# Optimization experiments

Measured on AMD Instinct MI355X. Metric: run time of the kernel, lower is better.

The kernel has to match this reference:

```python
import jax, jax.numpy as jnp
import numpy as np

B, S, D, H, HD = 2, 2048, 1024, 16, 64


def setup_inputs() -> dict:
    key = jax.random.key(0)
    ks = jax.random.split(key, 11)
    scale_in = 1.0 / np.sqrt(D)
    return {
        "query": jax.random.normal(ks[0], (B, S, D), jnp.float32),
        "key": jax.random.normal(ks[1], (B, S, D), jnp.float32),
        "value": jax.random.normal(ks[2], (B, S, D), jnp.float32),
        "Wq": jax.random.normal(ks[3], (H, D, HD), jnp.float32) * scale_in,
        "bq": jax.random.normal(ks[4], (H, HD), jnp.float32) * 0.02,
        "Wk": jax.random.normal(ks[5], (H, D, HD), jnp.float32) * scale_in,
        "bk": jax.random.normal(ks[6], (H, HD), jnp.float32) * 0.02,
        "Wv": jax.random.normal(ks[7], (H, D, HD), jnp.float32) * scale_in,
        "bv": jax.random.normal(ks[8], (H, HD), jnp.float32) * 0.02,
        "Wo": jax.random.normal(ks[9], (D, D), jnp.float32) * scale_in,
        "bo": jax.random.normal(ks[10], (D,), jnp.float32) * 0.02,
    }


def reference(query, key, value, Wq, bq, Wk, bk, Wv, bv, Wo, bo):
    # Per-head projections, batched over heads (equivalent to the ModuleList loop).
    q = jnp.einsum('bsd,hdk->bhsk', query, Wq) + bq[None, :, None, :]   # [B,H,S,HD]
    k = jnp.einsum('bsd,hdk->bhsk', key, Wk) + bk[None, :, None, :]
    v = jnp.einsum('bsd,hdk->bhsk', value, Wv) + bv[None, :, None, :]
    scale = 1.0 / jnp.sqrt(jnp.asarray(q.shape[-1], q.dtype))
    scores = jnp.einsum('bhsk,bhtk->bhst', q, k) * scale                # [B,H,S,S]
    attn = jax.nn.softmax(scores, axis=-1)
    ctx = jnp.einsum('bhst,bhtk->bhsk', attn, v)                        # [B,H,S,HD]
    # Concat heads along last dim: [B,S,H*HD] == [B,S,D]
    x = jnp.transpose(ctx, (0, 2, 1, 3)).reshape(ctx.shape[0], ctx.shape[2], -1)
    return x @ Wo + bo
```

## Files before the change

kernel.cpp:

```cpp
#include <hip/hip_runtime.h>
#include <hip/hip_bf16.h>

typedef __bf16 bf16;
typedef __bf16 bf16x8 __attribute__((ext_vector_type(8)));
typedef __bf16 bf16x4 __attribute__((ext_vector_type(4)));
typedef __bf16 bf16x2 __attribute__((ext_vector_type(2)));
typedef float floatx4 __attribute__((ext_vector_type(4)));
typedef float floatx16 __attribute__((ext_vector_type(16)));
typedef int intx4 __attribute__((ext_vector_type(4)));

#define B_SZ 2
#define S_LEN 2048
#define D_DIM 1024
#define H_CNT 16
#define HD_DIM 64
#define M_ROWS 4096
#define QSCALE 0.18033688011112042f

__device__ __forceinline__ void async_ld16(const bf16* g, bf16* s) {
    __builtin_amdgcn_global_load_lds((const __attribute__((address_space(1))) void*)g,
                                     (__attribute__((address_space(3))) void*)s, 16, 0, 0);
}

__device__ __forceinline__ floatx4 mfma16(bf16x8 a, bf16x8 b, floatx4 c) {
    return __builtin_amdgcn_mfma_f32_16x16x32_bf16(a, b, c, 0, 0, 0);
}
__device__ __forceinline__ floatx16 mfma32(bf16x8 a, bf16x8 b, floatx16 c) {
    return __builtin_amdgcn_mfma_f32_32x32x16_bf16(a, b, c, 0, 0, 0);
}

__device__ __forceinline__ bf16x8 mkfrag(int a0, int a1, int b0, int b1) {
    asm("v_permlane32_swap_b32 %0, %1" : "+v"(a0), "+v"(b0));
    asm("v_permlane32_swap_b32 %0, %1" : "+v"(a1), "+v"(b1));
    intx4 q = {a0, a1, b0, b1};
    return __builtin_bit_cast(bf16x8, q);
}

struct PrepArgs {
    const float* cast_src[3]; bf16* cast_dst[3];
    const float* w_src[3];    bf16* w_dst[3];
    const float* wo;          bf16* wo_t;
};
__global__ __launch_bounds__(256) void prep(PrepArgs a) {
    __shared__ bf16 tile[32][33];
    const int bx = blockIdx.x, tid = threadIdx.x;
    if (bx < 12288) {
        const int t = bx >> 12, blk = bx & 4095;
        const float* s = a.cast_src[t];
        bf16* d = a.cast_dst[t];
        size_t i = ((size_t)blk * 256 + tid) * 4;
        float4 v = *(const float4*)(s + i);
        bf16x4 o = { (bf16)v.x, (bf16)v.y, (bf16)v.z, (bf16)v.w };
        *(bf16x4*)(d + i) = o;
        return;
    }
    int tx = tid & 31, ty = tid >> 5;
    const float* src; bf16* dst; int r0, c0, C, R;
    if (bx < 15360) {
        int idx = bx - 12288;
        int z = idx >> 6, xy = idx & 63;
        int mat = z >> 4, head = z & 15;
        src = a.w_src[mat] + (size_t)head * D_DIM * HD_DIM;
        dst = a.w_dst[mat] + (size_t)head * D_DIM * HD_DIM;
        r0 = (xy & 31) * 32; c0 = (xy >> 5) * 32; C = HD_DIM; R = D_DIM;
    } else {
        int idx = bx - 15360;
        src = a.wo; dst = a.wo_t;
        r0 = (idx & 31) * 32; c0 = (idx >> 5) * 32; C = D_DIM; R = D_DIM;
    }
#pragma unroll
    for (int i = 0; i < 32; i += 8)
        tile[ty + i][tx] = (bf16)src[(size_t)(r0 + ty + i) * C + c0 + tx];
    __syncthreads();
#pragma unroll
    for (int i = 0; i < 32; i += 8)
        dst[(size_t)(c0 + ty + i) * R + r0 + tx] = tile[tx][ty + i];
}

struct GemmPtrs { const bf16* A; const bf16* BT; const float* bias; bf16* C;
                  float scale; int mode; };
struct GemmArgs { GemmPtrs p[3]; };

__global__ __launch_bounds__(256) void gemm_bt(GemmArgs args) {
    __shared__ __align__(16) bf16 As[128 * 32];
    __shared__ __align__(16) bf16 Bs[128 * 32];
    const GemmPtrs P = args.p[blockIdx.z];
    const int tid = threadIdx.x, wave = tid >> 6, lane = tid & 63;
    const int quad = lane >> 4, l15 = lane & 15;
    const int bm = blockIdx.x * 128, bn = blockIdx.y * 128;
    const int wm = (wave >> 1) * 64, wn = (wave & 1) * 64;

    floatx4 acc[4][4];
#pragma unroll
    for (int i = 0; i < 4; i++)
#pragma unroll
        for (int j = 0; j < 4; j++) acc[i][j] = (floatx4){0.f, 0.f, 0.f, 0.f};

    const int srow = (lane >> 2);
    const int scol = (((lane & 3) ^ ((srow >> 1) & 3)) << 3);
    const int ck = ((quad ^ ((l15 >> 1) & 3)) << 3);
    for (int k0 = 0; k0 < 1024; k0 += 32) {
#pragma unroll
        for (int it = 0; it < 2; ++it) {
            int issue = it * 4 + wave;
            int row = issue * 16 + srow;
            async_ld16(P.A + (size_t)(bm + row) * 1024 + k0 + scol, &As[issue * 512]);
            async_ld16(P.BT + (size_t)(bn + row) * 1024 + k0 + scol, &Bs[issue * 512]);
        }
        __syncthreads();
        bf16x8 af[4], bfr[4];
#pragma unroll
        for (int mi = 0; mi < 4; mi++)
            af[mi] = *(const bf16x8*)&As[(wm + mi * 16 + l15) * 32 + ck];
#pragma unroll
        for (int ni = 0; ni < 4; ni++)
            bfr[ni] = *(const bf16x8*)&Bs[(wn + ni * 16 + l15) * 32 + ck];
#pragma unroll
        for (int mi = 0; mi < 4; mi++)
#pragma unroll
            for (int ni = 0; ni < 4; ni++) acc[mi][ni] = mfma16(af[mi], bfr[ni], acc[mi][ni]);
        __syncthreads();
    }
#pragma unroll
    for (int ni = 0; ni < 4; ni++) {
        int col = bn + wn + ni * 16 + l15;
        float bb = P.bias[col];
#pragma unroll
        for (int mi = 0; mi < 4; mi++) {
#pragma unroll
            for (int r = 0; r < 4; r++) {
                int row = bm + wm + mi * 16 + quad * 4 + r;
                float v = (acc[mi][ni][r] + bb) * P.scale;
                int b = row >> 11, s2 = row & 2047, h = col >> 6, hd = col & 63;
                if (P.mode == 1)
                    P.C[(((size_t)(b * H_CNT + h)) * S_LEN + s2) * HD_DIM + hd] = (bf16)v;
                else
                    P.C[(((size_t)(b * H_CNT + h)) * HD_DIM + hd) * S_LEN + s2] = (bf16)v;
            }
        }
    }
}

__global__ __launch_bounds__(256) void gemm_out64(const bf16* __restrict__ A,
                                                  const bf16* __restrict__ BT,
                                                  const float* __restrict__ bias,
                                                  float* __restrict__ Cf) {
    __shared__ __align__(16) bf16 As[64 * 32];
    __shared__ __align__(16) bf16 Bs[64 * 32];
    const int tid = threadIdx.x, wave = tid >> 6, lane = tid & 63;
    const int quad = lane >> 4, l15 = lane & 15;
    const int bm = blockIdx.x * 64, bn = blockIdx.y * 64;
    const int wm = (wave >> 1) * 32, wn = (wave & 1) * 32;

    floatx4 acc[2][2];
#pragma unroll
    for (int i = 0; i < 2; i++)
#pragma unroll
        for (int j = 0; j < 2; j++) acc[i][j] = (floatx4){0.f, 0.f, 0.f, 0.f};

    const int srow = (lane >> 2);
    const int scol = (((lane & 3) ^ ((srow >> 1) & 3)) << 3);
    const int ck = ((quad ^ ((l15 >> 1) & 3)) << 3);
    for (int k0 = 0; k0 < 1024; k0 += 32) {
        {
            int row = wave * 16 + srow;
            async_ld16(A  + (size_t)(bm + row) * 1024 + k0 + scol, &As[wave * 512]);
            async_ld16(BT + (size_t)(bn + row) * 1024 + k0 + scol, &Bs[wave * 512]);
        }
        __syncthreads();
        bf16x8 af[2], bfr[2];
#pragma unroll
        for (int mi = 0; mi < 2; mi++)
            af[mi] = *(const bf16x8*)&As[(wm + mi * 16 + l15) * 32 + ck];
#pragma unroll
        for (int ni = 0; ni < 2; ni++)
            bfr[ni] = *(const bf16x8*)&Bs[(wn + ni * 16 + l15) * 32 + ck];
#pragma unroll
        for (int mi = 0; mi < 2; mi++)
#pragma unroll
            for (int ni = 0; ni < 2; ni++) acc[mi][ni] = mfma16(af[mi], bfr[ni], acc[mi][ni]);
        __syncthreads();
    }
#pragma unroll
    for (int ni = 0; ni < 2; ni++) {
        int col = bn + wn + ni * 16 + l15;
        float bb = bias[col];
#pragma unroll
        for (int mi = 0; mi < 2; mi++) {
#pragma unroll
            for (int r = 0; r < 4; r++) {
                int row = bm + wm + mi * 16 + quad * 4 + r;
                Cf[(size_t)row * 1024 + col] = acc[mi][ni][r] + bb;
            }
        }
    }
}

__global__ __launch_bounds__(512, 4) void attn(const bf16* __restrict__ Qg, const bf16* __restrict__ Kg,
                                               const bf16* __restrict__ Vtg, bf16* __restrict__ ctx) {
    __shared__ __align__(16) bf16 smem[32768];
    const int tid = threadIdx.x, wave = tid >> 6, lane = tid & 63;
    const int l31 = lane & 31, half = lane >> 5;
    const int grp = wave >> 2, wg = wave & 3;
    const int bid = blockIdx.x;
    const int bh = (bid >> 1) & 31;
    const int qb = ((bid >> 6) << 1) | (bid & 1);
    const int q0blk = qb * 128;
    const bf16* Kp = Kg + (size_t)bh * S_LEN * HD_DIM;
    const bf16* Vp = Vtg + (size_t)bh * HD_DIM * S_LEN;
    const int tbase = grp * 1024;

    const int f0 = wg * 512 + lane * 8, f1 = (wg + 4) * 512 + lane * 8;
    const int kc0 = f0 >> 9, kt0 = (f0 >> 3) & 63;
    const int kc1 = f1 >> 9, kt1 = (f1 >> 3) & 63;
    bf16* const Kbase = smem + grp * 8192;
    bf16* const Vbase = smem + 16384 + grp * 8192;

#define STAGE(BUF, T0) do { \
        bf16* Kd = Kbase + (BUF) * 4096; \
        bf16* Vd = Vbase + (BUF) * 4096; \
        async_ld16(Kp + (size_t)((T0) + kt0) * HD_DIM + kc0 * 8, Kd + wg * 512); \
        async_ld16(Kp + (size_t)((T0) + kt1) * HD_DIM + kc1 * 8, Kd + (wg + 4) * 512); \
        async_ld16(Vp + (size_t)kt0 * S_LEN + (T0) + kc0 * 8, Vd + wg * 512); \
        async_ld16(Vp + (size_t)kt1 * S_LEN + (T0) + kc1 * 8, Vd + (wg + 4) * 512); \
    } while (0)

    STAGE(0, tbase);
    bf16x8 qf[4];
    {
        const bf16* qrow = Qg + ((size_t)bh * S_LEN + q0blk + wg * 32 + l31) * HD_DIM;
#pragma unroll
        for (int kb = 0; kb < 4; ++kb)
            qf[kb] = *(const bf16x8*)(qrow + (2 * kb + half) * 8);
    }
    __syncthreads();

    float l_i = 0.f;
    floatx16 o0 = {0}, o1 = {0};

    for (int rd = 0; rd < 16; ++rd) {
        const int cur = rd & 1;
        if (rd < 15) STAGE(cur ^ 1, tbase + (rd + 1) * 64);
        const bf16* Kt = Kbase + cur * 4096;
        const bf16* Vt = Vbase + cur * 4096;
        floatx16 sc0 = {0}, sc1 = {0};
        __builtin_amdgcn_s_setprio(1);
#pragma unroll
        for (int kb = 0; kb < 4; ++kb) {
            bf16x8 k0 = *(const bf16x8*)&Kt[(2 * kb + half) * 512 + l31 * 8];
            bf16x8 k1 = *(const bf16x8*)&Kt[(2 * kb + half) * 512 + (32 + l31) * 8];
            sc0 = mfma32(k0, qf[kb], sc0);
            sc1 = mfma32(k1, qf[kb], sc1);
        }
        __builtin_amdgcn_s_setprio(0);
        float rs = 0.f;
        int w0[8], w1[8];
#pragma unroll
        for (int e = 0; e < 16; e += 2) {
            float p0 = __builtin_amdgcn_exp2f(sc0[e]);
            float p1 = __builtin_amdgcn_exp2f(sc0[e + 1]);
            rs += p0 + p1;
            bf16x2 t2 = {(bf16)p0, (bf16)p1};
            w0[e >> 1] = __builtin_bit_cast(int, t2);
        }
#pragma unroll
        for (int e = 0; e < 16; e += 2) {
            float p0 = __builtin_amdgcn_exp2f(sc1[e]);
            float p1 = __builtin_amdgcn_exp2f(sc1[e + 1]);
            rs += p0 + p1;
            bf16x2 t2 = {(bf16)p0, (bf16)p1};
            w1[e >> 1] = __builtin_bit_cast(int, t2);
        }
        l_i += rs;
        bf16x8 pfr[4];
        pfr[0] = mkfrag(w0[0], w0[1], w0[2], w0[3]);
        pfr[1] = mkfrag(w0[4], w0[5], w0[6], w0[7]);
        pfr[2] = mkfrag(w1[0], w1[1], w1[2], w1[3]);
        pfr[3] = mkfrag(w1[4], w1[5], w1[6], w1[7]);
        __builtin_amdgcn_s_setprio(1);
#pragma unroll
        for (int kb = 0; kb < 4; ++kb) {
            bf16x8 v0 = *(const bf16x8*)&Vt[(2 * kb + half) * 512 + l31 * 8];
            bf16x8 v1 = *(const bf16x8*)&Vt[(2 * kb + half) * 512 + (32 + l31) * 8];
            o0 = mfma32(v0, pfr[kb], o0);
            o1 = mfma32(v1, pfr[kb], o1);
        }
        __builtin_amdgcn_s_setprio(0);
        __syncthreads();
    }
#undef STAGE

    l_i += __shfl_xor(l_i, 32);

    float* slabF = (float*)smem;
    float* lA = slabF + 4 * 2112;
    if (grp == 0) {
        float* S0 = slabF + wg * 2112;
#pragma unroll
        for (int s2 = 0; s2 < 2; ++s2) {
            const floatx16 oo = s2 ? o1 : o0;
#pragma unroll
            for (int e = 0; e < 16; ++e) {
                int hd = s2 * 32 + (e & 3) + 8 * (e >> 2) + 4 * half;
                S0[l31 * 66 + hd] = oo[e];
            }
        }
        if (lane < 32) lA[wg * 32 + l31] = l_i;
    }
    __syncthreads();
    if (grp == 1) {
        float* S0 = slabF + wg * 2112;
        float lt = l_i + lA[wg * 32 + l31];
        float inv = 1.f / lt;
        int b = bh >> 4, hh = bh & 15;
        bf16* Sw = smem + 17408 + wg * 1280;
#pragma unroll
        for (int s2 = 0; s2 < 2; ++s2) {
            const floatx16 oo = s2 ? o1 : o0;
#pragma unroll
            for (int e = 0; e < 16; ++e) {
                int hd = (e & 3) + 8 * (e >> 2) + 4 * half;
                float v = (oo[e] + S0[l31 * 66 + s2 * 32 + hd]) * inv;
                Sw[l31 * 40 + hd] = (bf16)v;
            }
#pragma unroll
            for (int p = 0; p < 2; ++p) {
                int q = p * 16 + (lane >> 2), part = lane & 3;
                bf16x8 v = *(const bf16x8*)&Sw[q * 40 + part * 8];
                int s = q0blk + wg * 32 + q;
                *(bf16x8*)&ctx[((size_t)(b * S_LEN + s)) * D_DIM + hh * 64 + s2 * 32 + part * 8] = v;
            }
        }
    }
}

extern "C" void kernel_launch(void* const* d_in, const int* in_sizes, int n_in,
                              void* d_out, int out_size, void* d_ws, size_t ws_size,
                              hipStream_t stream) {
    const float* query = (const float*)d_in[0];
    const float* key   = (const float*)d_in[1];
    const float* value = (const float*)d_in[2];
    const float* Wq = (const float*)d_in[3];
    const float* bq = (const float*)d_in[4];
    const float* Wk = (const float*)d_in[5];
    const float* bk = (const float*)d_in[6];
    const float* Wv = (const float*)d_in[7];
    const float* bv = (const float*)d_in[8];
    const float* Wo = (const float*)d_in[9];
    const float* bo = (const float*)d_in[10];
    float* out = (float*)d_out;

    bf16* ws = (bf16*)d_ws;
    const size_t ASZ = (size_t)M_ROWS * D_DIM;
    const size_t WSZ = (size_t)H_CNT * D_DIM * HD_DIM;
    const size_t TSZ = (size_t)B_SZ * H_CNT * S_LEN * HD_DIM;
    bf16* Qc  = ws;
    bf16* Kc  = Qc + ASZ;
    bf16* Vc  = Kc + ASZ;
    bf16* WqT = Vc + ASZ;
    bf16* WkT = WqT + WSZ;
    bf16* WvT = WkT + WSZ;
    bf16* WoT = WvT + WSZ;
    bf16* Qb  = WoT + (size_t)D_DIM * D_DIM;
    bf16* Kb  = Qb + TSZ;
    bf16* Vtb = Kb + TSZ;
    bf16* ctx = Vtb + TSZ;

    dim3 blk(256);

    PrepArgs pa;
    pa.cast_src[0] = query; pa.cast_src[1] = key; pa.cast_src[2] = value;
    pa.cast_dst[0] = Qc;    pa.cast_dst[1] = Kc;  pa.cast_dst[2] = Vc;
    pa.w_src[0] = Wq; pa.w_src[1] = Wk; pa.w_src[2] = Wv;
    pa.w_dst[0] = WqT; pa.w_dst[1] = WkT; pa.w_dst[2] = WvT;
    pa.wo = Wo; pa.wo_t = WoT;
    prep<<<dim3(16384), blk, 0, stream>>>(pa);

    GemmArgs qkv;
    qkv.p[0] = {Qc, WqT, bq, Qb, QSCALE, 1};
    qkv.p[1] = {Kc, WkT, bk, Kb, 1.0f, 1};
    qkv.p[2] = {Vc, WvT, bv, Vtb, 1.0f, 2};
    gemm_bt<<<dim3(32, 8, 3), blk, 0, stream>>>(qkv);

    attn<<<dim3(512), dim3(512), 0, stream>>>(Qb, Kb, Vtb, ctx);

    gemm_out64<<<dim3(64, 16), blk, 0, stream>>>(ctx, WoT, bo, out);
}
```

Baseline: 218.5 us.

## Fuse fp32-to-bf16 activation cast into QKV GEMM tile loads

New measurement: 226.3 us. 3.6% more time.

```diff
diff --git a/kernel.cpp b/kernel.cpp
--- a/kernel.cpp
+++ b/kernel.cpp
@@ -17,7 +17,7 @@
 #define M_ROWS 4096
 #define QSCALE 0.18033688011112042f
 
-__device__ __forceinline__ void async_ld16(const bf16* g, bf16* s) {
+__device__ __forceinline__ void async_ld16(const void* g, void* s) {
     __builtin_amdgcn_global_load_lds((const __attribute__((address_space(1))) void*)g,
                                      (__attribute__((address_space(3))) void*)s, 16, 0, 0);
 }
@@ -37,34 +37,22 @@
 }
 
 struct PrepArgs {
-    const float* cast_src[3]; bf16* cast_dst[3];
     const float* w_src[3];    bf16* w_dst[3];
     const float* wo;          bf16* wo_t;
 };
 __global__ __launch_bounds__(256) void prep(PrepArgs a) {
     __shared__ bf16 tile[32][33];
     const int bx = blockIdx.x, tid = threadIdx.x;
-    if (bx < 12288) {
-        const int t = bx >> 12, blk = bx & 4095;
-        const float* s = a.cast_src[t];
-        bf16* d = a.cast_dst[t];
-        size_t i = ((size_t)blk * 256 + tid) * 4;
-        float4 v = *(const float4*)(s + i);
-        bf16x4 o = { (bf16)v.x, (bf16)v.y, (bf16)v.z, (bf16)v.w };
-        *(bf16x4*)(d + i) = o;
-        return;
-    }
     int tx = tid & 31, ty = tid >> 5;
     const float* src; bf16* dst; int r0, c0, C, R;
-    if (bx < 15360) {
-        int idx = bx - 12288;
-        int z = idx >> 6, xy = idx & 63;
+    if (bx < 3072) {
+        int z = bx >> 6, xy = bx & 63;
         int mat = z >> 4, head = z & 15;
         src = a.w_src[mat] + (size_t)head * D_DIM * HD_DIM;
         dst = a.w_dst[mat] + (size_t)head * D_DIM * HD_DIM;
         r0 = (xy & 31) * 32; c0 = (xy >> 5) * 32; C = HD_DIM; R = D_DIM;
     } else {
-        int idx = bx - 15360;
+        int idx = bx - 3072;
         src = a.wo; dst = a.wo_t;
         r0 = (idx & 31) * 32; c0 = (idx >> 5) * 32; C = D_DIM; R = D_DIM;
     }
@@ -77,12 +65,12 @@
         dst[(size_t)(c0 + ty + i) * R + r0 + tx] = tile[tx][ty + i];
 }
 
-struct GemmPtrs { const bf16* A; const bf16* BT; const float* bias; bf16* C;
+struct GemmPtrs { const float* Af; const bf16* BT; const float* bias; bf16* C;
                   float scale; int mode; };
 struct GemmArgs { GemmPtrs p[3]; };
 
 __global__ __launch_bounds__(256) void gemm_bt(GemmArgs args) {
-    __shared__ __align__(16) bf16 As[128 * 32];
+    __shared__ __align__(16) float As[128 * 32];
     __shared__ __align__(16) bf16 Bs[128 * 32];
     const GemmPtrs P = args.p[blockIdx.z];
     const int tid = threadIdx.x, wave = tid >> 6, lane = tid & 63;
@@ -99,19 +87,33 @@
     const int srow = (lane >> 2);
     const int scol = (((lane & 3) ^ ((srow >> 1) & 3)) << 3);
     const int ck = ((quad ^ ((l15 >> 1) & 3)) << 3);
+    const int arl = lane >> 3, apos = lane & 7;
+
     for (int k0 = 0; k0 < 1024; k0 += 32) {
+#pragma unroll
+        for (int it = 0; it < 4; ++it) {
+            int i = it * 4 + wave;
+            int row = i * 8 + arl;
+            int c = apos ^ (row & 7);
+            async_ld16(P.Af + (size_t)(bm + row) * 1024 + k0 + c * 4, &As[i * 256]);
+        }
 #pragma unroll
         for (int it = 0; it < 2; ++it) {
             int issue = it * 4 + wave;
             int row = issue * 16 + srow;
-            async_ld16(P.A + (size_t)(bm + row) * 1024 + k0 + scol, &As[issue * 512]);
             async_ld16(P.BT + (size_t)(bn + row) * 1024 + k0 + scol, &Bs[issue * 512]);
         }
         __syncthreads();
         bf16x8 af[4], bfr[4];
 #pragma unroll
-        for (int mi = 0; mi < 4; mi++)
-            af[mi] = *(const bf16x8*)&As[(wm + mi * 16 + l15) * 32 + ck];
+        for (int mi = 0; mi < 4; mi++) {
+            int r = wm + mi * 16 + l15;
+            int p0 = (2 * quad) ^ (r & 7), p1 = (2 * quad + 1) ^ (r & 7);
+            float4 f0 = *(const float4*)&As[r * 32 + p0 * 4];
+            float4 f1 = *(const float4*)&As[r * 32 + p1 * 4];
+            af[mi] = (bf16x8){(bf16)f0.x, (bf16)f0.y, (bf16)f0.z, (bf16)f0.w,
+                              (bf16)f1.x, (bf16)f1.y, (bf16)f1.z, (bf16)f1.w};
+        }
 #pragma unroll
         for (int ni = 0; ni < 4; ni++)
             bfr[ni] = *(const bf16x8*)&Bs[(wn + ni * 16 + l15) * 32 + ck];
@@ -351,13 +353,9 @@
     float* out = (float*)d_out;
 
     bf16* ws = (bf16*)d_ws;
-    const size_t ASZ = (size_t)M_ROWS * D_DIM;
     const size_t WSZ = (size_t)H_CNT * D_DIM * HD_DIM;
     const size_t TSZ = (size_t)B_SZ * H_CNT * S_LEN * HD_DIM;
-    bf16* Qc  = ws;
-    bf16* Kc  = Qc + ASZ;
-    bf16* Vc  = Kc + ASZ;
-    bf16* WqT = Vc + ASZ;
+    bf16* WqT = ws;
     bf16* WkT = WqT + WSZ;
     bf16* WvT = WkT + WSZ;
     bf16* WoT = WvT + WSZ;
@@ -369,17 +367,15 @@
     dim3 blk(256);
 
     PrepArgs pa;
-    pa.cast_src[0] = query; pa.cast_src[1] = key; pa.cast_src[2] = value;
-    pa.cast_dst[0] = Qc;    pa.cast_dst[1] = Kc;  pa.cast_dst[2] = Vc;
     pa.w_src[0] = Wq; pa.w_src[1] = Wk; pa.w_src[2] = Wv;
     pa.w_dst[0] = WqT; pa.w_dst[1] = WkT; pa.w_dst[2] = WvT;
     pa.wo = Wo; pa.wo_t = WoT;
-    prep<<<dim3(16384), blk, 0, stream>>>(pa);
+    prep<<<dim3(4096), blk, 0, stream>>>(pa);
 
     GemmArgs qkv;
-    qkv.p[0] = {Qc, WqT, bq, Qb, QSCALE, 1};
-    qkv.p[1] = {Kc, WkT, bk, Kb, 1.0f, 1};
-    qkv.p[2] = {Vc, WvT, bv, Vtb, 1.0f, 2};
+    qkv.p[0] = {query, WqT, bq, Qb, QSCALE, 1};
+    qkv.p[1] = {key,   WkT, bk, Kb, 1.0f, 1};
+    qkv.p[2] = {value, WvT, bv, Vtb, 1.0f, 2};
     gemm_bt<<<dim3(32, 8, 3), blk, 0, stream>>>(qkv);
 
     attn<<<dim3(512), dim3(512), 0, stream>>>(Qb, Kb, Vtb, ctx);
```
